# Performance work log

Measured on AMD Instinct MI355X. Metric: run time of the kernel, lower is better.

Reference implementation:

```python
import jax, jax.numpy as jnp
import numpy as np

BLOCK_SIZE = 256
N_EMBD = 384
NUM_BLOCKS = 3
N_HEADS = 6
VOCAB_SIZE = 65
HEAD = N_EMBD // N_HEADS
EPS = 1e-5


def setup_inputs() -> dict:
    key = jax.random.key(0)
    ks = jax.random.split(key, 20)
    B, T = 64, 256
    s = 0.02
    L = NUM_BLOCKS
    inp = {
        "idx": jax.random.randint(ks[0], (B, T), 0, VOCAB_SIZE),
        "tok_emb": jax.random.normal(ks[1], (VOCAB_SIZE, N_EMBD), jnp.float32) * s,
        "pos_emb": jax.random.normal(ks[2], (BLOCK_SIZE, N_EMBD), jnp.float32) * s,
        "Wq": jax.random.normal(ks[3], (L, N_EMBD, N_EMBD), jnp.float32) * s,
        "Wk": jax.random.normal(ks[4], (L, N_EMBD, N_EMBD), jnp.float32) * s,
        "Wv": jax.random.normal(ks[5], (L, N_EMBD, N_EMBD), jnp.float32) * s,
        "Wo": jax.random.normal(ks[6], (L, N_EMBD, N_EMBD), jnp.float32) * s,
        "bo": jnp.zeros((L, N_EMBD), jnp.float32),
        "ln1_g": jnp.ones((L, N_EMBD), jnp.float32),
        "ln1_b": jnp.zeros((L, N_EMBD), jnp.float32),
        "ln2_g": jnp.ones((L, N_EMBD), jnp.float32),
        "ln2_b": jnp.zeros((L, N_EMBD), jnp.float32),
        "W1": jax.random.normal(ks[7], (L, N_EMBD, 4 * N_EMBD), jnp.float32) * s,
        "b1": jnp.zeros((L, 4 * N_EMBD), jnp.float32),
        "W2": jax.random.normal(ks[8], (L, 4 * N_EMBD, N_EMBD), jnp.float32) * s,
        "b2": jnp.zeros((L, N_EMBD), jnp.float32),
        "lnf_g": jnp.ones((N_EMBD,), jnp.float32),
        "lnf_b": jnp.zeros((N_EMBD,), jnp.float32),
        "Wlm": jax.random.normal(ks[9], (N_EMBD, VOCAB_SIZE), jnp.float32) * s,
        "blm": jnp.zeros((VOCAB_SIZE,), jnp.float32),
    }
    return inp


def _ln(x, g, b):
    m = jnp.mean(x, axis=-1, keepdims=True)
    v = jnp.mean((x - m) ** 2, axis=-1, keepdims=True)
    return (x - m) * jax.lax.rsqrt(v + EPS) * g + b


def reference(idx, tok_emb, pos_emb, Wq, Wk, Wv, Wo, bo, ln1_g, ln1_b,
              ln2_g, ln2_b, W1, b1, W2, b2, lnf_g, lnf_b, Wlm, blm):
    B, T = idx.shape
    x = tok_emb[idx] + pos_emb[:T]  # [B,T,C]
    scale = N_EMBD ** (-0.5)  # NOTE: original scales by full C=N_EMBD, not head_size
    causal = jnp.tril(jnp.ones((T, T), bool))
    neg_inf = jnp.finfo(x.dtype).min
    for l in range(NUM_BLOCKS):
        h = _ln(x, ln1_g[l], ln1_b[l])
        q = (h @ Wq[l]).reshape(B, T, N_HEADS, HEAD)
        k = (h @ Wk[l]).reshape(B, T, N_HEADS, HEAD)
        v = (h @ Wv[l]).reshape(B, T, N_HEADS, HEAD)
        wei = jnp.einsum("bthd,bshd->bhts", q, k) * scale
        wei = jnp.where(causal, wei, neg_inf)
        wei = jax.nn.softmax(wei, axis=-1)  # dropout is identity in eval
        att = jnp.einsum("bhts,bshd->bthd", wei, v).reshape(B, T, N_EMBD)
        x = x + att @ Wo[l] + bo[l]
        h2 = _ln(x, ln2_g[l], ln2_b[l])
        x = x + jax.nn.relu(h2 @ W1[l] + b1[l]) @ W2[l] + b2[l]
    x = _ln(x, lnf_g, lnf_b)
    logits = x @ Wlm + blm  # [B,T,V]
    return logits
```

## Files before the change

### kernel.cpp

```cpp
#include <hip/hip_runtime.h>

#define Bb 64
#define Tt 256
#define Cc 384
#define Ll 3
#define Hh 6
#define HD 64
#define Vv 65
#define FF 1536
#define NT (Bb*Tt)
#define CQ 1152
#define LDP 72

typedef unsigned short u16;
typedef unsigned int   u32;
typedef __attribute__((ext_vector_type(8))) short bf16x8;
typedef __attribute__((ext_vector_type(4))) float f32x4;

__device__ __forceinline__ float bf2f(u16 u) {
    u32 v = ((u32)u) << 16; float f; __builtin_memcpy(&f, &v, 4); return f;
}
__device__ __forceinline__ u16 f2bf(float f) {
    u32 u; __builtin_memcpy(&u, &f, 4);
    u = (u + 0x7fffu + ((u >> 16) & 1u)) >> 16;
    return (u16)u;
}
__device__ __forceinline__ void gload16(const void* g, void* l) {
    __builtin_amdgcn_global_load_lds(
        (const __attribute__((address_space(1))) u32*)g,
        (__attribute__((address_space(3))) u32*)l, 16, 0, 0);
}

__global__ __launch_bounds__(256) void k_embed_ln(const int* __restrict__ idx,
    const float* __restrict__ tok, const float* __restrict__ pos,
    const float* __restrict__ g, const float* __restrict__ b,
    float* __restrict__ x, u16* __restrict__ h)
{
    int bt   = (int)((blockIdx.x * 256 + threadIdx.x) >> 6);
    int lane = threadIdx.x & 63;
    int t = bt % Tt;
    const float2* tr = (const float2*)(tok + (long)idx[bt] * Cc);
    const float2* pr = (const float2*)(pos + (long)t * Cc);
    float2 v[3]; float s = 0.f;
    #pragma unroll
    for (int j = 0; j < 3; ++j) {
        int c = lane + 64 * j;
        float2 tv = tr[c], pv = pr[c];
        v[j].x = tv.x + pv.x; v[j].y = tv.y + pv.y;
        s += v[j].x + v[j].y;
    }
    float2* xr = (float2*)(x + (long)bt * Cc);
    #pragma unroll
    for (int j = 0; j < 3; ++j) xr[lane + 64 * j] = v[j];
    #pragma unroll
    for (int m = 32; m; m >>= 1) s += __shfl_xor(s, m, 64);
    float mean = s * (1.f / 384.f);
    float q = 0.f;
    #pragma unroll
    for (int j = 0; j < 3; ++j) {
        float dx = v[j].x - mean, dy = v[j].y - mean;
        q += dx * dx + dy * dy;
    }
    #pragma unroll
    for (int m = 32; m; m >>= 1) q += __shfl_xor(q, m, 64);
    float rstd = rsqrtf(q * (1.f / 384.f) + 1e-5f);
    u32* hr = (u32*)(h + (long)bt * Cc);
    const float2* gr = (const float2*)g;
    const float2* br = (const float2*)b;
    #pragma unroll
    for (int j = 0; j < 3; ++j) {
        int c = lane + 64 * j;
        float2 gv = gr[c], bv = br[c];
        u32 lo = f2bf((v[j].x - mean) * rstd * gv.x + bv.x);
        u32 hi = f2bf((v[j].y - mean) * rstd * gv.y + bv.y);
        hr[c] = lo | (hi << 16);
    }
}

__global__ __launch_bounds__(256) void k_ln(const float* __restrict__ x,
    const float* __restrict__ g, const float* __restrict__ b, u16* __restrict__ h)
{
    int row  = (int)((blockIdx.x * 256 + threadIdx.x) >> 6);
    int lane = threadIdx.x & 63;
    const float2* xr = (const float2*)(x + (long)row * Cc);
    float2 v[3]; float s = 0.f;
    #pragma unroll
    for (int j = 0; j < 3; ++j) { v[j] = xr[lane + 64 * j]; s += v[j].x + v[j].y; }
    #pragma unroll
    for (int m = 32; m; m >>= 1) s += __shfl_xor(s, m, 64);
    float mean = s * (1.f / 384.f);
    float q = 0.f;
    #pragma unroll
    for (int j = 0; j < 3; ++j) {
        float dx = v[j].x - mean, dy = v[j].y - mean;
        q += dx * dx + dy * dy;
    }
    #pragma unroll
    for (int m = 32; m; m >>= 1) q += __shfl_xor(q, m, 64);
    float rstd = rsqrtf(q * (1.f / 384.f) + 1e-5f);
    u32* hr = (u32*)(h + (long)row * Cc);
    const float2* gr = (const float2*)g;
    const float2* br = (const float2*)b;
    #pragma unroll
    for (int j = 0; j < 3; ++j) {
        int c = lane + 64 * j;
        float2 gv = gr[c], bv = br[c];
        u32 lo = f2bf((v[j].x - mean) * rstd * gv.x + bv.x);
        u32 hi = f2bf((v[j].y - mean) * rstd * gv.y + bv.y);
        hr[c] = lo | (hi << 16);
    }
}

__global__ __launch_bounds__(256) void k_cvtT_all(
    const float* __restrict__ Wq, const float* __restrict__ Wk,
    const float* __restrict__ Wv, const float* __restrict__ Wo,
    const float* __restrict__ W1, const float* __restrict__ W2,
    u16* __restrict__ Wqkvt, u16* __restrict__ Wot,
    u16* __restrict__ W1t, u16* __restrict__ W2t)
{
    int t = blockIdx.x;
    const float* src; u16* dst; int K, N, tt;
    if (t < 1728) {
        int m = t / 144; tt = t % 144; K = Cc; N = Cc;
        if (m < 9) {
            int l = m / 3, q = m % 3;
            src = (q == 0 ? Wq : q == 1 ? Wk : Wv) + (size_t)l * Cc * Cc;
            dst = Wqkvt + (size_t)l * CQ * Cc + (size_t)q * Cc * Cc;
        } else {
            int l = m - 9;
            src = Wo + (size_t)l * Cc * Cc;
            dst = Wot + (size_t)l * Cc * Cc;
        }
    } else if (t < 3456) {
        int u = t - 1728; int l = u / 576; tt = u % 576; K = Cc; N = FF;
        src = W1 + (size_t)l * Cc * FF; dst = W1t + (size_t)l * FF * Cc;
    } else {
        int u = t - 3456; int l = u / 576; tt = u % 576; K = FF; N = Cc;
        src = W2 + (size_t)l * FF * Cc; dst = W2t + (size_t)l * Cc * FF;
    }
    int nk = K / 32;
    int kt = (tt % nk) * 32, nt = (tt / nk) * 32;
    __shared__ u16 tile[32][33];
    int tx = threadIdx.x & 31, ty = threadIdx.x >> 5;
    #pragma unroll
    for (int r = 0; r < 4; ++r)
        tile[ty + 8 * r][tx] = f2bf(src[(long)(kt + ty + 8 * r) * N + nt + tx]);
    __syncthreads();
    #pragma unroll
    for (int r = 0; r < 4; ++r)
        dst[(long)(nt + ty + 8 * r) * K + kt + tx] = tile[tx][ty + 8 * r];
}

__global__ void k_cvtT_lm(const float* __restrict__ W, u16* __restrict__ Wt)
{
    int i = blockIdx.x * 256 + threadIdx.x;
    if (i >= 128 * Cc) return;
    int k = i % Cc, n = i / Cc;
    Wt[i] = (n < Vv) ? f2bf(W[(long)k * Vv + n]) : (u16)0;
}

template<int EPI>
__global__ __launch_bounds__(256) void k_gemm128(
    const u16* __restrict__ A, const u16* __restrict__ Bt,
    const float* __restrict__ bias, void* __restrict__ Cout, int M, int N, int K)
{
    __shared__ __align__(16) u16 As[2][128 * 64];
    __shared__ __align__(16) u16 Bs[2][128 * 64];
    const int bm = blockIdx.x * 128;
    const int bn = blockIdx.y * 128;
    const int tid = threadIdx.x;
    const int lane = tid & 63, w = tid >> 6;
    const int wr = w >> 1, wc = w & 1;
    const int l15 = lane & 15, g = lane >> 4;
    const int lr = lane >> 3;
    const int lc = ((lane & 7) ^ lr) * 8;

    f32x4 acc[4][4] = {};
    const u16* Ag = A  + (long)(bm + w * 32 + lr) * K + lc;
    const u16* Bg = Bt + (long)(bn + w * 32 + lr) * K + lc;

    auto stage = [&](int buf, int k0) {
        u16* Ad = As[buf] + (w * 4) * 512;
        u16* Bd = Bs[buf] + (w * 4) * 512;
        #pragma unroll
        for (int s = 0; s < 4; ++s) {
            gload16(Ag + (long)s * 8 * K + k0, Ad + s * 512);
            gload16(Bg + (long)s * 8 * K + k0, Bd + s * 512);
        }
    };
    const int nt = K / 64;
    stage(0, 0);
    if (nt > 1) stage(1, 64);
    for (int t = 0; t < nt; ++t) {
        if (t < nt - 1) asm volatile("s_waitcnt vmcnt(8)" ::: "memory");
        else            asm volatile("s_waitcnt vmcnt(0)" ::: "memory");
        __builtin_amdgcn_s_barrier();
        asm volatile("" ::: "memory");
        const char* Abuf = (const char*)As[t & 1];
        const char* Bbuf = (const char*)Bs[t & 1];
        #pragma unroll
        for (int hh = 0; hh < 2; ++hh) {
            const int cs = hh * 4 + g;
            bf16x8 af[4], bfr[4];
            #pragma unroll
            for (int mi = 0; mi < 4; ++mi) {
                int row = wr * 64 + mi * 16 + l15;
                af[mi] = *(const bf16x8*)(Abuf + row * 128 + ((cs ^ (row & 7)) << 4));
            }
            #pragma unroll
            for (int ni = 0; ni < 4; ++ni) {
                int row = wc * 64 + ni * 16 + l15;
                bfr[ni] = *(const bf16x8*)(Bbuf + row * 128 + ((cs ^ (row & 7)) << 4));
            }
            #pragma unroll
            for (int mi = 0; mi < 4; ++mi)
            #pragma unroll
            for (int ni = 0; ni < 4; ++ni)
                acc[mi][ni] = __builtin_amdgcn_mfma_f32_16x16x32_bf16(af[mi], bfr[ni], acc[mi][ni], 0, 0, 0);
        }
        asm volatile("" ::: "memory");
        __builtin_amdgcn_s_barrier();
        if (t + 2 < nt) stage(t & 1, (t + 2) * 64);
    }
    #pragma unroll
    for (int mi = 0; mi < 4; ++mi)
    #pragma unroll
    for (int ni = 0; ni < 4; ++ni)
    #pragma unroll
    for (int i = 0; i < 4; ++i) {
        int row = bm + wr * 64 + mi * 16 + g * 4 + i;
        int col = bn + wc * 64 + ni * 16 + l15;
        float v = acc[mi][ni][i];
        if constexpr (EPI == 1) v = fmaxf(v + bias[col], 0.f);
        ((u16*)Cout)[(long)row * N + col] = f2bf(v);
    }
}

template<int EPI, int PIPE>
__global__ __launch_bounds__(256) void k_gemm_n64(
    const u16* __restrict__ A, const u16* __restrict__ Bt,
    const float* __restrict__ bias, const float* __restrict__ R,
    void* __restrict__ Cout, int M, int N, int K, int Nout)
{
    __shared__ __align__(16) u16 As[PIPE ? 2 : 1][128 * 64];
    __shared__ __align__(16) u16 Bs[PIPE ? 2 : 1][64 * 64];
    const int bm = blockIdx.x * 128;
    const int bn = blockIdx.y * 64;
    const int tid = threadIdx.x;
    const int lane = tid & 63, w = tid >> 6;
    const int l15 = lane & 15, g = lane >> 4;
    const int lr = lane >> 3;
    const int lc = ((lane & 7) ^ lr) * 8;

    f32x4 acc[2][4] = {};
    const u16* Ag = A  + (long)(bm + w * 32 + lr) * K + lc;
    const u16* Bg = Bt + (long)(bn + w * 16 + lr) * K + lc;

    auto stage = [&](int buf, int k0) {
        u16* Ad = As[buf] + (w * 4) * 512;
        u16* Bd = Bs[buf] + (w * 2) * 512;
        #pragma unroll
        for (int s = 0; s < 4; ++s)
            gload16(Ag + (long)s * 8 * K + k0, Ad + s * 512);
        #pragma unroll
        for (int t = 0; t < 2; ++t)
            gload16(Bg + (long)t * 8 * K + k0, Bd + t * 512);
    };

    auto compute = [&](int buf) {
        const char* Abuf = (const char*)As[buf];
        const char* Bbuf = (const char*)Bs[buf];
        #pragma unroll
        for (int hh = 0; hh < 2; ++hh) {
            const int cs = hh * 4 + g;
            bf16x8 af[2], bfr[4];
            #pragma unroll
            for (int mi = 0; mi < 2; ++mi) {
                int row = w * 32 + mi * 16 + l15;
                af[mi] = *(const bf16x8*)(Abuf + row * 128 + ((cs ^ (row & 7)) << 4));
            }
            #pragma unroll
            for (int ni = 0; ni < 4; ++ni) {
                int row = ni * 16 + l15;
                bfr[ni] = *(const bf16x8*)(Bbuf + row * 128 + ((cs ^ (row & 7)) << 4));
            }
            #pragma unroll
            for (int mi = 0; mi < 2; ++mi)
            #pragma unroll
            for (int ni = 0; ni < 4; ++ni)
                acc[mi][ni] = __builtin_amdgcn_mfma_f32_16x16x32_bf16(af[mi], bfr[ni], acc[mi][ni], 0, 0, 0);
        }
    };

    if constexpr (PIPE == 0) {
        for (int k0 = 0; k0 < K; k0 += 64) {
            stage(0, k0);
            __syncthreads();
            compute(0);
            __syncthreads();
        }
    } else {
        const int nt = K / 64;
        stage(0, 0);
        if (nt > 1) stage(1, 64);
        for (int t = 0; t < nt; ++t) {
            if (t < nt - 1) asm volatile("s_waitcnt vmcnt(6)" ::: "memory");
            else            asm volatile("s_waitcnt vmcnt(0)" ::: "memory");
            __builtin_amdgcn_s_barrier();
            asm volatile("" ::: "memory");
            compute(t & 1);
            asm volatile("" ::: "memory");
            __builtin_amdgcn_s_barrier();
            if (t + 2 < nt) stage(t & 1, (t + 2) * 64);
        }
    }
    #pragma unroll
    for (int mi = 0; mi < 2; ++mi)
    #pragma unroll
    for (int ni = 0; ni < 4; ++ni)
    #pragma unroll
    for (int i = 0; i < 4; ++i) {
        int row = bm + w * 32 + mi * 16 + g * 4 + i;
        int col = bn + ni * 16 + l15;
        float v = acc[mi][ni][i];
        if constexpr (EPI == 2) {
            long o = (long)row * N + col;
            ((float*)Cout)[o] = v + bias[col] + R[o];
        } else {
            if (col < Nout)
                ((float*)Cout)[(long)row * Nout + col] = v + bias[col];
        }
    }
}

__global__ __launch_bounds__(256) void k_attn_mfma(const u16* __restrict__ qkv,
                                                   u16* __restrict__ att)
{
    __shared__ __align__(16) u16 ks[64][LDP];
    __shared__ __align__(16) u16 vt[64][LDP];
    __shared__ __align__(16) u16 pt[4][16][LDP];
    const int qt = blockIdx.x, hh = blockIdx.y, b = blockIdx.z;
    const int tid = threadIdx.x, lane = tid & 63, w = tid >> 6;
    const int l15 = lane & 15, g = lane >> 4;
    const int q0 = qt * 64;
    const long tokbase = (long)b * Tt;
    const float scale = 0.051031036307982884f;

    bf16x8 qa0, qa1;
    {
        const u16* qp = qkv + (tokbase + q0 + w * 16 + l15) * CQ + hh * HD + g * 8;
        qa0 = *(const bf16x8*)(qp);
        qa1 = *(const bf16x8*)(qp + 32);
    }
    f32x4 o[4] = {};
    float mrow[4] = {-1e30f, -1e30f, -1e30f, -1e30f};
    float lrow[4] = {0.f, 0.f, 0.f, 0.f};

    for (int kt = 0; kt <= qt; ++kt) {
        {
            int key = tid >> 2, c0 = (tid & 3) * 16;
            const u16* kg = qkv + (tokbase + kt * 64 + key) * CQ + Cc     + hh * HD + c0;
            const u16* vg = qkv + (tokbase + kt * 64 + key) * CQ + 2 * Cc + hh * HD + c0;
            *(bf16x8*)&ks[key][c0]     = *(const bf16x8*)kg;
            *(bf16x8*)&ks[key][c0 + 8] = *(const bf16x8*)(kg + 8);
            bf16x8 v0 = *(const bf16x8*)vg;
            bf16x8 v1 = *(const bf16x8*)(vg + 8);
            #pragma unroll
            for (int j = 0; j < 8; ++j) vt[c0 + j][key]     = (u16)v0[j];
            #pragma unroll
            for (int j = 0; j < 8; ++j) vt[c0 + 8 + j][key] = (u16)v1[j];
        }
        __syncthreads();
        f32x4 s[4] = {};
        #pragma unroll
        for (int c = 0; c < 4; ++c) {
            bf16x8 kb0 = *(const bf16x8*)&ks[c * 16 + l15][g * 8];
            bf16x8 kb1 = *(const bf16x8*)&ks[c * 16 + l15][32 + g * 8];
            s[c] = __builtin_amdgcn_mfma_f32_16x16x32_bf16(qa0, kb0, s[c], 0, 0, 0);
            s[c] = __builtin_amdgcn_mfma_f32_16x16x32_bf16(qa1, kb1, s[c], 0, 0, 0);
        }
        const bool diag = (kt == qt);
        #pragma unroll
        for (int c = 0; c < 4; ++c)
        #pragma unroll
        for (int i = 0; i < 4; ++i) {
            float v = s[c][i] * scale;
            if (diag && (c * 16 + l15 > w * 16 + 4 * g + i)) v = -1e30f;
            s[c][i] = v;
        }
        #pragma unroll
        for (int i = 0; i < 4; ++i) {
            float m0 = fmaxf(fmaxf(s[0][i], s[1][i]), fmaxf(s[2][i], s[3][i]));
            #pragma unroll
            for (int mm = 1; mm < 16; mm <<= 1) m0 = fmaxf(m0, __shfl_xor(m0, mm, 64));
            float mn = fmaxf(mrow[i], m0);
            float alpha = __expf(mrow[i] - mn);
            mrow[i] = mn;
            float sum = 0.f;
            #pragma unroll
            for (int c = 0; c < 4; ++c) {
                float p = __expf(s[c][i] - mn);
                s[c][i] = p;
                sum += p;
            }
            #pragma unroll
            for (int mm = 1; mm < 16; mm <<= 1) sum += __shfl_xor(sum, mm, 64);
            lrow[i] = lrow[i] * alpha + sum;
            #pragma unroll
            for (int d = 0; d < 4; ++d) o[d][i] *= alpha;
        }
        #pragma unroll
        for (int c = 0; c < 4; ++c)
        #pragma unroll
        for (int i = 0; i < 4; ++i)
            pt[w][g * 4 + i][c * 16 + l15] = f2bf(s[c][i]);
        bf16x8 pa0 = *(const bf16x8*)&pt[w][l15][g * 8];
        bf16x8 pa1 = *(const bf16x8*)&pt[w][l15][32 + g * 8];
        #pragma unroll
        for (int d = 0; d < 4; ++d) {
            bf16x8 vb0 = *(const bf16x8*)&vt[d * 16 + l15][g * 8];
            bf16x8 vb1 = *(const bf16x8*)&vt[d * 16 + l15][32 + g * 8];
            o[d] = __builtin_amdgcn_mfma_f32_16x16x32_bf16(pa0, vb0, o[d], 0, 0, 0);
            o[d] = __builtin_amdgcn_mfma_f32_16x16x32_bf16(pa1, vb1, o[d], 0, 0, 0);
        }
        __syncthreads();
    }
    #pragma unroll
    for (int i = 0; i < 4; ++i) {
        float inv = 1.f / lrow[i];
        int row = q0 + w * 16 + g * 4 + i;
        u16* ap = att + (tokbase + row) * Cc + hh * HD;
        #pragma unroll
        for (int d = 0; d < 4; ++d)
            ap[d * 16 + l15] = f2bf(o[d][i] * inv);
    }
}

extern "C" void kernel_launch(void* const* d_in, const int* in_sizes, int n_in,
                              void* d_out, int out_size, void* d_ws, size_t ws_size,
                              hipStream_t stream)
{
    (void)in_sizes; (void)n_in; (void)out_size; (void)ws_size;
    const int*   idx  = (const int*)d_in[0];
    const float* tok  = (const float*)d_in[1];
    const float* pos  = (const float*)d_in[2];
    const float* Wq   = (const float*)d_in[3];
    const float* Wk   = (const float*)d_in[4];
    const float* Wv   = (const float*)d_in[5];
    const float* Wo   = (const float*)d_in[6];
    const float* bo   = (const float*)d_in[7];
    const float* ln1g = (const float*)d_in[8];
    const float* ln1b = (const float*)d_in[9];
    const float* ln2g = (const float*)d_in[10];
    const float* ln2b = (const float*)d_in[11];
    const float* W1   = (const float*)d_in[12];
    const float* b1   = (const float*)d_in[13];
    const float* W2   = (const float*)d_in[14];
    const float* b2   = (const float*)d_in[15];
    const float* lnfg = (const float*)d_in[16];
    const float* lnfb = (const float*)d_in[17];
    const float* Wlm  = (const float*)d_in[18];
    const float* blm  = (const float*)d_in[19];

    char* w = (char*)d_ws;
    auto carve = [&](size_t bytes) { char* p = w; w += (bytes + 255) & ~(size_t)255; return p; };
    float* x   = (float*)carve((size_t)NT * Cc * 4);
    u16*  big  = (u16*)carve((size_t)NT * FF * 2);
    u16*  h    = (u16*)carve((size_t)NT * Cc * 2);
    u16*  ab   = (u16*)carve((size_t)NT * Cc * 2);
    u16*  Wqkvt= (u16*)carve((size_t)Ll * CQ * Cc * 2);
    u16*  Wot  = (u16*)carve((size_t)Ll * Cc * Cc * 2);
    u16*  W1t  = (u16*)carve((size_t)Ll * FF * Cc * 2);
    u16*  W2t  = (u16*)carve((size_t)Ll * Cc * FF * 2);
    u16*  Wlmt = (u16*)carve((size_t)128 * Cc * 2);
    u16*  qkvb = big;
    u16*  fb   = big;

    const int TPB = 256;
    k_cvtT_all<<<5184, TPB, 0, stream>>>(Wq, Wk, Wv, Wo, W1, W2, Wqkvt, Wot, W1t, W2t);
    k_cvtT_lm<<<(128 * Cc + 255) / 256, TPB, 0, stream>>>(Wlm, Wlmt);
    k_embed_ln<<<NT / 4, TPB, 0, stream>>>(idx, tok, pos, ln1g, ln1b, x, h);

    for (int l = 0; l < Ll; ++l) {
        if (l > 0)
            k_ln<<<NT / 4, TPB, 0, stream>>>(x, ln1g + l * Cc, ln1b + l * Cc, h);
        k_gemm128<0><<<dim3(NT / 128, CQ / 128), TPB, 0, stream>>>(
            h, Wqkvt + (size_t)l * CQ * Cc, nullptr, qkvb, NT, CQ, Cc);
        k_attn_mfma<<<dim3(4, Hh, Bb), TPB, 0, stream>>>(qkvb, ab);
        k_gemm_n64<2, 0><<<dim3(NT / 128, Cc / 64), TPB, 0, stream>>>(
            ab, Wot + (size_t)l * Cc * Cc, bo + l * Cc, x, x, NT, Cc, Cc, Cc);
        k_ln<<<NT / 4, TPB, 0, stream>>>(x, ln2g + l * Cc, ln2b + l * Cc, h);
        k_gemm128<1><<<dim3(NT / 128, FF / 128), TPB, 0, stream>>>(
            h, W1t + (size_t)l * FF * Cc, b1 + l * FF, fb, NT, FF, Cc);
        k_gemm_n64<2, 1><<<dim3(NT / 128, Cc / 64), TPB, 0, stream>>>(
            fb, W2t + (size_t)l * Cc * FF, b2 + l * Cc, x, x, NT, Cc, FF, Cc);
    }
    k_ln<<<NT / 4, TPB, 0, stream>>>(x, lnfg, lnfb, h);
    k_gemm_n64<3, 0><<<dim3(NT / 128, 2), TPB, 0, stream>>>(
        h, Wlmt, blm, nullptr, (float*)d_out, NT, 128, Cc, Vv);
}
```

Baseline: 454.2 us.

## Add XCD-aware workgroup swizzle to GEMMs and drop double-buffered n64 pipeline

Remaps the linear workgroup id so consecutive tiles land on the same XCD, which should raise L2 reuse of shared A/B tiles across the eight chiplets. The swizzle is applied to both the 128x128 GEMM and the N=64 GEMM. Separately, the N=64 GEMM loses its double-buffered LDS pipeline, so the FFN down-projection now runs single-buffered with two barriers per K step. That lowers LDS use and may raise occupancy, but it gives up load/compute overlap for the K=1536 GEMM. The swizzle formula assumes the workgroup count divides by 8, which holds for these grids.

```diff
diff --git a/kernel.cpp b/kernel.cpp
--- a/kernel.cpp
+++ b/kernel.cpp
@@ -29,6 +29,9 @@
     __builtin_amdgcn_global_load_lds(
         (const __attribute__((address_space(1))) u32*)g,
         (__attribute__((address_space(3))) u32*)l, 16, 0, 0);
+}
+__device__ __forceinline__ int xcd_swz(int orig, int nwg) {
+    return (orig & 7) * (nwg >> 3) + (orig >> 3);
 }
 
 __global__ __launch_bounds__(256) void k_embed_ln(const int* __restrict__ idx,
@@ -166,8 +169,10 @@
 {
     __shared__ __align__(16) u16 As[2][128 * 64];
     __shared__ __align__(16) u16 Bs[2][128 * 64];
-    const int bm = blockIdx.x * 128;
-    const int bn = blockIdx.y * 128;
+    const int nwg = gridDim.x * gridDim.y;
+    const int swz = xcd_swz(blockIdx.x + blockIdx.y * gridDim.x, nwg);
+    const int bm = (swz % gridDim.x) * 128;
+    const int bn = (swz / gridDim.x) * 128;
     const int tid = threadIdx.x;
     const int lane = tid & 63, w = tid >> 6;
     const int wr = w >> 1, wc = w & 1;
@@ -236,16 +241,18 @@
     }
 }
 
-template<int EPI, int PIPE>
+template<int EPI>
 __global__ __launch_bounds__(256) void k_gemm_n64(
     const u16* __restrict__ A, const u16* __restrict__ Bt,
     const float* __restrict__ bias, const float* __restrict__ R,
     void* __restrict__ Cout, int M, int N, int K, int Nout)
 {
-    __shared__ __align__(16) u16 As[PIPE ? 2 : 1][128 * 64];
-    __shared__ __align__(16) u16 Bs[PIPE ? 2 : 1][64 * 64];
-    const int bm = blockIdx.x * 128;
-    const int bn = blockIdx.y * 64;
+    __shared__ __align__(16) u16 As[128 * 64];
+    __shared__ __align__(16) u16 Bs[64 * 64];
+    const int nwg = gridDim.x * gridDim.y;
+    const int swz = xcd_swz(blockIdx.x + blockIdx.y * gridDim.x, nwg);
+    const int bm = (swz % gridDim.x) * 128;
+    const int bn = (swz / gridDim.x) * 64;
     const int tid = threadIdx.x;
     const int lane = tid & 63, w = tid >> 6;
     const int l15 = lane & 15, g = lane >> 4;
@@ -255,21 +262,17 @@
     f32x4 acc[2][4] = {};
     const u16* Ag = A  + (long)(bm + w * 32 + lr) * K + lc;
     const u16* Bg = Bt + (long)(bn + w * 16 + lr) * K + lc;
-
-    auto stage = [&](int buf, int k0) {
-        u16* Ad = As[buf] + (w * 4) * 512;
-        u16* Bd = Bs[buf] + (w * 2) * 512;
+    u16* Ad = As + (w * 4) * 512;
+    u16* Bd = Bs + (w * 2) * 512;
+
+    for (int k0 = 0; k0 < K; k0 += 64) {
         #pragma unroll
         for (int s = 0; s < 4; ++s)
             gload16(Ag + (long)s * 8 * K + k0, Ad + s * 512);
         #pragma unroll
         for (int t = 0; t < 2; ++t)
             gload16(Bg + (long)t * 8 * K + k0, Bd + t * 512);
-    };
-
-    auto compute = [&](int buf) {
-        const char* Abuf = (const char*)As[buf];
-        const char* Bbuf = (const char*)Bs[buf];
+        __syncthreads();
         #pragma unroll
         for (int hh = 0; hh < 2; ++hh) {
             const int cs = hh * 4 + g;
@@ -277,12 +280,12 @@
             #pragma unroll
             for (int mi = 0; mi < 2; ++mi) {
                 int row = w * 32 + mi * 16 + l15;
-                af[mi] = *(const bf16x8*)(Abuf + row * 128 + ((cs ^ (row & 7)) << 4));
+                af[mi] = *(const bf16x8*)((const char*)As + row * 128 + ((cs ^ (row & 7)) << 4));
             }
             #pragma unroll
             for (int ni = 0; ni < 4; ++ni) {
                 int row = ni * 16 + l15;
-                bfr[ni] = *(const bf16x8*)(Bbuf + row * 128 + ((cs ^ (row & 7)) << 4));
+                bfr[ni] = *(const bf16x8*)((const char*)Bs + row * 128 + ((cs ^ (row & 7)) << 4));
             }
             #pragma unroll
             for (int mi = 0; mi < 2; ++mi)
@@ -290,29 +293,7 @@
             for (int ni = 0; ni < 4; ++ni)
                 acc[mi][ni] = __builtin_amdgcn_mfma_f32_16x16x32_bf16(af[mi], bfr[ni], acc[mi][ni], 0, 0, 0);
         }
-    };
-
-    if constexpr (PIPE == 0) {
-        for (int k0 = 0; k0 < K; k0 += 64) {
-            stage(0, k0);
-            __syncthreads();
-            compute(0);
-            __syncthreads();
-        }
-    } else {
-        const int nt = K / 64;
-        stage(0, 0);
-        if (nt > 1) stage(1, 64);
-        for (int t = 0; t < nt; ++t) {
-            if (t < nt - 1) asm volatile("s_waitcnt vmcnt(6)" ::: "memory");
-            else            asm volatile("s_waitcnt vmcnt(0)" ::: "memory");
-            __builtin_amdgcn_s_barrier();
-            asm volatile("" ::: "memory");
-            compute(t & 1);
-            asm volatile("" ::: "memory");
-            __builtin_amdgcn_s_barrier();
-            if (t + 2 < nt) stage(t & 1, (t + 2) * 64);
-        }
+        __syncthreads();
     }
     #pragma unroll
     for (int mi = 0; mi < 2; ++mi)
@@ -487,15 +468,15 @@
         k_gemm128<0><<<dim3(NT / 128, CQ / 128), TPB, 0, stream>>>(
             h, Wqkvt + (size_t)l * CQ * Cc, nullptr, qkvb, NT, CQ, Cc);
         k_attn_mfma<<<dim3(4, Hh, Bb), TPB, 0, stream>>>(qkvb, ab);
-        k_gemm_n64<2, 0><<<dim3(NT / 128, Cc / 64), TPB, 0, stream>>>(
+        k_gemm_n64<2><<<dim3(NT / 128, Cc / 64), TPB, 0, stream>>>(
             ab, Wot + (size_t)l * Cc * Cc, bo + l * Cc, x, x, NT, Cc, Cc, Cc);
         k_ln<<<NT / 4, TPB, 0, stream>>>(x, ln2g + l * Cc, ln2b + l * Cc, h);
         k_gemm128<1><<<dim3(NT / 128, FF / 128), TPB, 0, stream>>>(
             h, W1t + (size_t)l * FF * Cc, b1 + l * FF, fb, NT, FF, Cc);
-        k_gemm_n64<2, 1><<<dim3(NT / 128, Cc / 64), TPB, 0, stream>>>(
+        k_gemm_n64<2><<<dim3(NT / 128, Cc / 64), TPB, 0, stream>>>(
             fb, W2t + (size_t)l * Cc * FF, b2 + l * Cc, x, x, NT, Cc, FF, Cc);
     }
     k_ln<<<NT / 4, TPB, 0, stream>>>(x, lnfg, lnfb, h);
-    k_gemm_n64<3, 0><<<dim3(NT / 128, 2), TPB, 0, stream>>>(
+    k_gemm_n64<3><<<dim3(NT / 128, 2), TPB, 0, stream>>>(
         h, Wlmt, blm, nullptr, (float*)d_out, NT, 128, Cc, Vv);
 }
```

After: 601.2 us. 1.32x slower.
